# Performance work log

Hardware: AMD Instinct MI355X
Metric: run time of the kernel (lower is better)

## Reference

```python
import jax, jax.numpy as jnp
import numpy as np

N = 3072          # num nodes
E = 49152         # num edges (avg degree 16)
D = 256           # hidden_dim
O = 512           # output_dim
H = 8             # num_heads
DH = D // H       # head_dim = 32
NET = 5           # num_edge_types
NC = 8            # num_communities
L_LOC = 2         # num_local_layers
L_GLB = 2         # num_global_layers


def _layernorm(x, g, b, eps=1e-5):
    m = jnp.mean(x, axis=-1, keepdims=True)
    v = jnp.mean((x - m) ** 2, axis=-1, keepdims=True)
    return (x - m) * jax.lax.rsqrt(v + eps) * g + b


def setup_inputs() -> dict:
    key = jax.random.key(0)
    ks = jax.random.split(key, 40)
    s = 0.02
    inp = {
        "x": jax.random.normal(ks[0], (N, 1), jnp.float32),
        "edge_index": jax.random.randint(ks[1], (2, E), 0, N),
        "edge_types": jax.random.randint(ks[2], (E,), 0, NET),
        "pos_encoding": jax.random.normal(ks[3], (N, D), jnp.float32),
        "community_ids": jax.random.randint(ks[4], (N,), 0, NC),
        "adj_matrix": jnp.zeros((N, N), jnp.float32),
        # node embedding Linear(1, D)
        "emb_w": jax.random.normal(ks[5], (1, D)) * s,
        "emb_b": jnp.zeros((D,)),
        # local (Graphormer) layers, stacked over L_LOC
        "loc_qw": jax.random.normal(ks[6], (L_LOC, D, D)) * s,
        "loc_qb": jnp.zeros((L_LOC, D)),
        "loc_kw": jax.random.normal(ks[7], (L_LOC, D, D)) * s,
        "loc_kb": jnp.zeros((L_LOC, D)),
        "loc_vw": jax.random.normal(ks[8], (L_LOC, D, D)) * s,
        "loc_vb": jnp.zeros((L_LOC, D)),
        "loc_ow": jax.random.normal(ks[9], (L_LOC, D, D)) * s,
        "loc_ob": jnp.zeros((L_LOC, D)),
        "loc_eb": jax.random.normal(ks[10], (L_LOC, NET, H)) * s,  # edge-type attn bias per head
        "loc_ln_g": jnp.ones((L_LOC, D)),
        "loc_ln_b": jnp.zeros((L_LOC, D)),
        # global interaction layers, stacked over L_GLB
        "glob_qw": jax.random.normal(ks[11], (L_GLB, D, D)) * s,
        "glob_qb": jnp.zeros((L_GLB, D)),
        "glob_kw": jax.random.normal(ks[12], (L_GLB, D, D)) * s,
        "glob_kb": jnp.zeros((L_GLB, D)),
        "glob_vw": jax.random.normal(ks[13], (L_GLB, D, D)) * s,
        "glob_vb": jnp.zeros((L_GLB, D)),
        "glob_ow": jax.random.normal(ks[14], (L_GLB, D, D)) * s,
        "glob_ob": jnp.zeros((L_GLB, D)),
        "glob_ln_g": jnp.ones((L_GLB, D)),
        "glob_ln_b": jnp.zeros((L_GLB, D)),
        # output projection
        "out_w": jax.random.normal(ks[15], (D, O)) * s,
        "out_b": jnp.zeros((O,)),
    }
    return inp


def reference(x, edge_index, edge_types, pos_encoding, community_ids, adj_matrix,
              emb_w, emb_b,
              loc_qw, loc_qb, loc_kw, loc_kb, loc_vw, loc_vb, loc_ow, loc_ob,
              loc_eb, loc_ln_g, loc_ln_b,
              glob_qw, glob_qb, glob_kw, glob_kb, glob_vw, glob_vb,
              glob_ow, glob_ob, glob_ln_g, glob_ln_b,
              out_w, out_b):
    n = x.shape[0]
    h = x @ emb_w + emb_b                                  # [N, D]
    same = community_ids[:, None] == community_ids[None, :]  # [N, N] same-community mask
    src, dst = edge_index[0], edge_index[1]

    # Local layers: the original per-community subgraph loop (with full attention
    # inside each community) is mathematically a single masked full attention
    # restricted to same-community pairs, with edge-type bias at graph edges.
    for l in range(loc_qw.shape[0]):
        hp = h + pos_encoding
        q = (hp @ loc_qw[l] + loc_qb[l]).reshape(n, H, DH)
        k = (hp @ loc_kw[l] + loc_kb[l]).reshape(n, H, DH)
        v = (hp @ loc_vw[l] + loc_vb[l]).reshape(n, H, DH)
        # edge-type attention bias, scattered at edges  -> [H, N, N]
        bias = jnp.zeros((H, n, n), dtype=h.dtype).at[:, src, dst].add(loc_eb[l][edge_types].T)
        scores = jnp.einsum('nhd,mhd->hnm', q, k) / np.sqrt(DH) + bias
        scores = jnp.where(same[None, :, :], scores, -jnp.inf)  # attend within community only
        attn = jax.nn.softmax(scores, axis=-1)
        o = jnp.einsum('hnm,mhd->nhd', attn, v).reshape(n, D)
        h = _layernorm(h + o @ loc_ow[l] + loc_ob[l], loc_ln_g[l], loc_ln_b[l])

    # Global interaction: attend only to nodes in *different* communities
    for g in range(glob_qw.shape[0]):
        Q = h @ glob_qw[g] + glob_qb[g]
        K = h @ glob_kw[g] + glob_kb[g]
        V = h @ glob_vw[g] + glob_vb[g]
        scores = (Q @ K.T) / np.sqrt(DH)                   # scaled by head_dim as in source
        scores = jnp.where(~same, scores, -jnp.inf)        # mask same-community (incl. self)
        attn = jax.nn.softmax(scores, axis=-1)
        o = (attn @ V) @ glob_ow[g] + glob_ob[g]
        h = _layernorm(o + h, glob_ln_g[g], glob_ln_b[g])

    return h @ out_w + out_b                               # [N, O]
```

## Files before the change

### kernel.cpp

```cpp
#include <hip/hip_runtime.h>
#include <hip/hip_bf16.h>
#include <stdint.h>

#define NN 3072
#define EE 49152
#define DD 256
#define OO 512
#define HH 8
#define DHH 32
#define NETT 5
#define NC 8
#define NCMAX 512
#define SCP 516
#define KS 16
#define NW 17

typedef __attribute__((ext_vector_type(8))) short short8;
typedef __attribute__((ext_vector_type(4))) float f32x4;

__device__ __forceinline__ short f2bf_s(float f){
    __hip_bfloat16 h = __float2bfloat16(f);
    return *reinterpret_cast<short*>(&h);
}
__device__ __forceinline__ float bf2f_s(short v){
    __hip_bfloat16 h;
    *reinterpret_cast<short*>(&h) = v;
    return __bfloat162float(h);
}

__global__ void k_embed(const float* __restrict__ x, const float* __restrict__ w,
                        const float* __restrict__ b, float* __restrict__ h){
    int i = blockIdx.x * 256 + threadIdx.x;
    int n = i >> 8, d = i & 255;
    h[i] = x[n] * w[d] + b[d];
}

__global__ __launch_bounds__(256) void k_vtrans(const float* __restrict__ v, short* __restrict__ vt){
    __shared__ float t[32][33];
    int bx = blockIdx.x;
    int by = blockIdx.y;
    int lx = threadIdx.x & 31, ly = threadIdx.x >> 5;
    for (int i = ly; i < 32; i += 8)
        t[i][lx] = v[(size_t)(bx * 32 + i) * DD + by * 32 + lx];
    __syncthreads();
    for (int r = ly; r < 32; r += 8)
        vt[(size_t)(by * 32 + r) * NN + bx * 32 + lx] = f2bf_s(t[lx][r]);
}

__global__ __launch_bounds__(256) void k_vtrans_sorted(const float* __restrict__ v,
                                                       const int* __restrict__ perm,
                                                       short* __restrict__ vt){
    __shared__ float t[32][33];
    int bx = blockIdx.x;
    int by = blockIdx.y;
    int lx = threadIdx.x & 31, ly = threadIdx.x >> 5;
    for (int i = ly; i < 32; i += 8)
        t[i][lx] = v[(size_t)perm[bx * 32 + i] * DD + by * 32 + lx];
    __syncthreads();
    for (int r = ly; r < 32; r += 8)
        vt[(size_t)(by * 32 + r) * NN + bx * 32 + lx] = f2bf_s(t[lx][r]);
}

struct WT {
    const float* src[NW];
    short*       dst[NW];
    int          M[NW];
};
__global__ __launch_bounds__(256) void k_wtrans(WT wt){
    int id = blockIdx.z;
    int M = wt.M[id];
    int bx = blockIdx.x;
    if (bx * 32 >= M) return;
    int by = blockIdx.y;
    __shared__ float t[32][33];
    int lx = threadIdx.x & 31, ly = threadIdx.x >> 5;
    const float* w = wt.src[id];
    for (int i = ly; i < 32; i += 8)
        t[i][lx] = w[(size_t)(by * 32 + i) * M + bx * 32 + lx];
    __syncthreads();
    short* d = wt.dst[id];
    for (int r = ly; r < 32; r += 8)
        d[(size_t)(bx * 32 + r) * DD + by * 32 + lx] = f2bf_s(t[lx][r]);
}

__global__ void k_count(const int* __restrict__ ei, int* __restrict__ cnt){
    int e = blockIdx.x * 256 + threadIdx.x;
    if (e < EE) atomicAdd(&cnt[ei[e]], 1);
}

__global__ void k_scan(const int* __restrict__ cnt, int* __restrict__ rp){
    __shared__ int part[256];
    int tid = threadIdx.x;
    int base = tid * 12;
    int loc[12]; int s = 0;
    for (int i = 0; i < 12; i++){ loc[i] = s; s += cnt[base + i]; }
    part[tid] = s; __syncthreads();
    if (tid == 0){ int a = 0; for (int i = 0; i < 256; i++){ int t = part[i]; part[i] = a; a += t; } }
    __syncthreads();
    int b = part[tid];
    for (int i = 0; i < 12; i++) rp[base + i] = b + loc[i];
    if (tid == 255) rp[NN] = b + s;
}

__global__ void k_fill(const int* __restrict__ ei, const int* __restrict__ et,
                       const int* __restrict__ rp, int* __restrict__ cur,
                       int* __restrict__ e_dst, int* __restrict__ e_typ){
    int e = blockIdx.x * 256 + threadIdx.x;
    if (e < EE){
        int s = ei[e], d = ei[EE + e];
        int p = atomicAdd(&cur[s], 1);
        int idx = rp[s] + p;
        e_dst[idx] = d; e_typ[idx] = et[e];
    }
}

__global__ void k_ccount(const int* __restrict__ comm, int* __restrict__ ccnt){
    int n = blockIdx.x * 256 + threadIdx.x;
    if (n < NN) atomicAdd(&ccnt[comm[n]], 1);
}

__global__ void k_cscan(const int* __restrict__ ccnt, int* __restrict__ cstart){
    cstart[0] = 0;
    for (int c = 0; c < NC; c++) cstart[c + 1] = cstart[c] + ccnt[c];
}

__global__ void k_cfill(const int* __restrict__ comm, const int* __restrict__ cstart,
                        int* __restrict__ ccur, int* __restrict__ perm, int* __restrict__ inv){
    int n = blockIdx.x * 256 + threadIdx.x;
    if (n < NN){
        int c = comm[n];
        int p = cstart[c] + atomicAdd(&ccur[c], 1);
        perm[p] = n; inv[n] = p;
    }
}

template<int M>
__global__ __launch_bounds__(256) void k_gemm_mfma(
        const float* __restrict__ A, const float* __restrict__ P,
        const short* __restrict__ Wt, const float* __restrict__ bias,
        float* __restrict__ C, short* __restrict__ Cbf){
    int tid = threadIdx.x;
    int w = tid >> 6, lane = tid & 63, quad = lane >> 4, col = lane & 15;
    int m0 = blockIdx.x * 64 + w * 16;
    int n0 = blockIdx.y * 64;

    const float* arow = A + (size_t)(m0 + col) * DD;
    const float* prow = P ? P + (size_t)(m0 + col) * DD : nullptr;

    f32x4 acc[4];
    #pragma unroll
    for (int su = 0; su < 4; su++) acc[su] = (f32x4){0.f, 0.f, 0.f, 0.f};

    #pragma unroll
    for (int f = 0; f < 8; f++){
        int k0 = f * 32 + quad * 8;
        float4 a0 = *(const float4*)(arow + k0);
        float4 a1 = *(const float4*)(arow + k0 + 4);
        if (P){
            float4 p0 = *(const float4*)(prow + k0);
            float4 p1 = *(const float4*)(prow + k0 + 4);
            a0.x += p0.x; a0.y += p0.y; a0.z += p0.z; a0.w += p0.w;
            a1.x += p1.x; a1.y += p1.y; a1.z += p1.z; a1.w += p1.w;
        }
        short8 af;
        af[0] = f2bf_s(a0.x); af[1] = f2bf_s(a0.y); af[2] = f2bf_s(a0.z); af[3] = f2bf_s(a0.w);
        af[4] = f2bf_s(a1.x); af[5] = f2bf_s(a1.y); af[6] = f2bf_s(a1.z); af[7] = f2bf_s(a1.w);
        #pragma unroll
        for (int su = 0; su < 4; su++){
            short8 bf = *(const short8*)(Wt + (size_t)(n0 + su * 16 + col) * DD + k0);
            acc[su] = __builtin_amdgcn_mfma_f32_16x16x32_bf16(af, bf, acc[su], 0, 0, 0);
        }
    }

    #pragma unroll
    for (int su = 0; su < 4; su++){
        int n = n0 + su * 16 + col;
        float bz = bias[n];
        #pragma unroll
        for (int r = 0; r < 4; r++){
            float val = acc[su][r] + bz;
            size_t idx = (size_t)(m0 + quad * 4 + r) * M + n;
            C[idx] = val;
            if (Cbf) Cbf[idx] = f2bf_s(val);
        }
    }
}

struct QKV {
    const short* Wt[3];
    const float* bias[3];
    float*       Cf[3];
    short*       Cb[3];
};
__global__ __launch_bounds__(256) void k_gemm_qkv(
        const float* __restrict__ A, const float* __restrict__ P,
        QKV q, const int* __restrict__ inv){
    int z = blockIdx.z;
    const short* Wt = q.Wt[z];
    const float* bias = q.bias[z];
    float* Cf = q.Cf[z];
    short* Cb = q.Cb[z];

    int tid = threadIdx.x;
    int w = tid >> 6, lane = tid & 63, quad = lane >> 4, col = lane & 15;
    int m0 = blockIdx.x * 64 + w * 16;
    int n0 = blockIdx.y * 64;

    const float* arow = A + (size_t)(m0 + col) * DD;
    const float* prow = P ? P + (size_t)(m0 + col) * DD : nullptr;

    f32x4 acc[4];
    #pragma unroll
    for (int su = 0; su < 4; su++) acc[su] = (f32x4){0.f, 0.f, 0.f, 0.f};

    #pragma unroll
    for (int f = 0; f < 8; f++){
        int k0 = f * 32 + quad * 8;
        float4 a0 = *(const float4*)(arow + k0);
        float4 a1 = *(const float4*)(arow + k0 + 4);
        if (P){
            float4 p0 = *(const float4*)(prow + k0);
            float4 p1 = *(const float4*)(prow + k0 + 4);
            a0.x += p0.x; a0.y += p0.y; a0.z += p0.z; a0.w += p0.w;
            a1.x += p1.x; a1.y += p1.y; a1.z += p1.z; a1.w += p1.w;
        }
        short8 af;
        af[0] = f2bf_s(a0.x); af[1] = f2bf_s(a0.y); af[2] = f2bf_s(a0.z); af[3] = f2bf_s(a0.w);
        af[4] = f2bf_s(a1.x); af[5] = f2bf_s(a1.y); af[6] = f2bf_s(a1.z); af[7] = f2bf_s(a1.w);
        #pragma unroll
        for (int su = 0; su < 4; su++){
            short8 bf = *(const short8*)(Wt + (size_t)(n0 + su * 16 + col) * DD + k0);
            acc[su] = __builtin_amdgcn_mfma_f32_16x16x32_bf16(af, bf, acc[su], 0, 0, 0);
        }
    }

    #pragma unroll
    for (int su = 0; su < 4; su++){
        int n = n0 + su * 16 + col;
        float bz = bias[n];
        #pragma unroll
        for (int r = 0; r < 4; r++){
            float val = acc[su][r] + bz;
            int m = m0 + quad * 4 + r;
            if (Cf) Cf[(size_t)m * DD + n] = val;
            if (Cb){
                int ms = inv ? inv[m] : m;
                Cb[(size_t)ms * DD + n] = f2bf_s(val);
            }
        }
    }
}

__global__ __launch_bounds__(256) void k_ln_res(float* __restrict__ h, const float* __restrict__ t,
                                                const float* __restrict__ g, const float* __restrict__ b){
    int n = blockIdx.x, d = threadIdx.x;
    __shared__ float red[256];
    float v = h[n * 256 + d] + t[n * 256 + d];
    red[d] = v; __syncthreads();
    for (int s = 128; s > 0; s >>= 1){ if (d < s) red[d] += red[d + s]; __syncthreads(); }
    float mean = red[0] * (1.0f / 256.0f); __syncthreads();
    float c = v - mean;
    red[d] = c * c; __syncthreads();
    for (int s = 128; s > 0; s >>= 1){ if (d < s) red[d] += red[d + s]; __syncthreads(); }
    float var = red[0] * (1.0f / 256.0f);
    h[n * 256 + d] = c * rsqrtf(var + 1e-5f) * g[d] + b[d];
}

__global__ __launch_bounds__(256) void k_local_attn6(
        const short* __restrict__ Qs, const short* __restrict__ Ks, const short* __restrict__ Vts,
        const int* __restrict__ cstart, const int* __restrict__ perm, const int* __restrict__ inv,
        const int* __restrict__ rp, const int* __restrict__ e_dst, const int* __restrict__ e_typ,
        const float* __restrict__ eb, float* __restrict__ o){
    int c  = blockIdx.y;
    int hh = blockIdx.z;
    int cs0 = cstart[c], cs1 = cstart[c + 1];
    int Nc = cs1 - cs0;
    int p0 = blockIdx.x * 16;
    if (p0 >= Nc) return;
    int tid = threadIdx.x;
    int w = tid >> 6, lane = tid & 63, quad = lane >> 4, col = lane & 15;
    int nt  = (Nc + 15) >> 4;
    int nt2 = (Nc + 31) >> 5;

    __shared__ float sc[16][SCP];
    __shared__ float linv[16];
    __shared__ int qnode[16];

    if (tid < 16) qnode[tid] = (p0 + tid < Nc) ? perm[cs0 + p0 + tid] : -1;

    int qrow = cs0 + min(p0 + col, Nc - 1);
    short8 qf = *(const short8*)(Qs + (size_t)qrow * DD + hh * DHH + quad * 8);

    const float scale = 0.17677669529663687f;

    for (int t = w; t < nt; t += 4){
        int kt = t * 16;
        int krow = cs0 + min(kt + col, Nc - 1);
        short8 kf = *(const short8*)(Ks + (size_t)krow * DD + hh * DHH + quad * 8);
        f32x4 s = __builtin_amdgcn_mfma_f32_16x16x32_bf16(qf, kf, (f32x4){0.f,0.f,0.f,0.f}, 0, 0, 0);
        #pragma unroll
        for (int r = 0; r < 4; r++)
            sc[quad * 4 + r][kt + col] = s[r] * scale;
    }
    __syncthreads();

    int qi = tid >> 4, l16 = tid & 15;
    {
        int n = qnode[qi];
        if (n >= 0){
            int re = rp[n + 1];
            for (int e2 = rp[n] + l16; e2 < re; e2 += 16){
                int dpos = inv[e_dst[e2]];
                if (dpos >= cs0 && dpos < cs1)
                    atomicAdd(&sc[qi][dpos - cs0], eb[e_typ[e2] * HH + hh]);
            }
        }
    }
    __syncthreads();

    {
        float lm = -1e30f;
        for (int m = l16; m < Nc; m += 16) lm = fmaxf(lm, sc[qi][m]);
        #pragma unroll
        for (int off = 1; off < 16; off <<= 1) lm = fmaxf(lm, __shfl_xor(lm, off));
        float ls = 0.f;
        for (int m = l16; m < Nc; m += 16){
            float e_ = __expf(sc[qi][m] - lm);
            sc[qi][m] = e_;
            ls += e_;
        }
        for (int m = (Nc & ~15) + l16; m < nt2 * 32; m += 16)
            if (m >= Nc) sc[qi][m] = 0.f;
        #pragma unroll
        for (int off = 1; off < 16; off <<= 1) ls += __shfl_xor(ls, off);
        if (l16 == 0) linv[qi] = 1.f / ls;
    }
    __syncthreads();

    f32x4 acc0 = (f32x4){0.f,0.f,0.f,0.f}, acc1 = (f32x4){0.f,0.f,0.f,0.f};
    for (int t2 = w; t2 < nt2; t2 += 4){
        int kt = t2 * 32;
        float4 pa = *(const float4*)&sc[col][kt + quad * 8];
        float4 pb = *(const float4*)&sc[col][kt + quad * 8 + 4];
        short8 pf;
        pf[0] = f2bf_s(pa.x); pf[1] = f2bf_s(pa.y); pf[2] = f2bf_s(pa.z); pf[3] = f2bf_s(pa.w);
        pf[4] = f2bf_s(pb.x); pf[5] = f2bf_s(pb.y); pf[6] = f2bf_s(pb.z); pf[7] = f2bf_s(pb.w);
        const short* vb0 = Vts + (size_t)(hh * DHH + col) * NN + cs0 + kt + quad * 8;
        short8 vf0 = *(const short8*)(vb0);
        short8 vf1 = *(const short8*)(vb0 + (size_t)16 * NN);
        acc0 = __builtin_amdgcn_mfma_f32_16x16x32_bf16(pf, vf0, acc0, 0, 0, 0);
        acc1 = __builtin_amdgcn_mfma_f32_16x16x32_bf16(pf, vf1, acc1, 0, 0, 0);
    }
    __syncthreads();
    {
        float (*pv)[16][33] = reinterpret_cast<float (*)[16][33]>(&sc[0][0]);
        #pragma unroll
        for (int r = 0; r < 4; r++){
            pv[w][quad * 4 + r][col]      = acc0[r];
            pv[w][quad * 4 + r][col + 16] = acc1[r];
        }
        __syncthreads();

        int q = tid >> 4, d0 = tid & 15;
        int n = qnode[q];
        #pragma unroll
        for (int half = 0; half < 2; half++){
            int dd = d0 + half * 16;
            float sum = pv[0][q][dd] + pv[1][q][dd] + pv[2][q][dd] + pv[3][q][dd];
            if (n >= 0) o[(size_t)n * DD + hh * DHH + dd] = sum * linv[q];
        }
    }
}

__global__ __launch_bounds__(256) void k_glob_mfma9(
        const short* __restrict__ Qb, const short* __restrict__ Kb,
        const short* __restrict__ Vt, const int* __restrict__ comm,
        short* __restrict__ Opart, float* __restrict__ lpart){
    int tid = threadIdx.x;
    int w = tid >> 6, lane = tid & 63, quad = lane >> 4, col = lane & 15;
    int qt = blockIdx.x * 64 + w * 16;
    int split = blockIdx.y;
    int ks0 = split * (NN / KS);

    __shared__ __align__(16) short Kl[32][264];
    __shared__ __align__(16) short Vl[256][40];
    __shared__ __align__(16) short Pl[4][16][40];

    short8 qf[8];
    #pragma unroll
    for (int f = 0; f < 8; f++)
        qf[f] = *(const short8*)(Qb + (size_t)(qt + col) * DD + f * 32 + quad * 8);

    int qc[4];
    #pragma unroll
    for (int r = 0; r < 4; r++) qc[r] = comm[qt + quad * 4 + r];

    f32x4 accO[16];
    #pragma unroll
    for (int dt = 0; dt < 16; dt++) accO[dt] = (f32x4){0.f, 0.f, 0.f, 0.f};
    float l_[4] = {0.f, 0.f, 0.f, 0.f};

    const float scale = 0.17677669529663687f;

    for (int t = 0; t < NN / KS / 32; t++){
        int kt = ks0 + t * 32;
        __syncthreads();
        #pragma unroll
        for (int i = 0; i < 4; i++){
            int idx = tid + i * 256;
            int row = idx >> 5, seg = idx & 31;
            *(short8*)&Kl[row][seg * 8] = *(const short8*)(Kb + (size_t)(kt + row) * DD + seg * 8);
        }
        #pragma unroll
        for (int i = 0; i < 4; i++){
            int idx = tid + i * 256;
            int d = idx >> 2, seg = idx & 3;
            *(short8*)&Vl[d][seg * 8] = *(const short8*)(Vt + (size_t)d * NN + kt + seg * 8);
        }
        __syncthreads();

        f32x4 s0 = (f32x4){0.f,0.f,0.f,0.f}, s1 = (f32x4){0.f,0.f,0.f,0.f};
        #pragma unroll
        for (int f = 0; f < 8; f++){
            short8 kf0 = *(const short8*)&Kl[col][f * 32 + quad * 8];
            short8 kf1 = *(const short8*)&Kl[16 + col][f * 32 + quad * 8];
            s0 = __builtin_amdgcn_mfma_f32_16x16x32_bf16(qf[f], kf0, s0, 0, 0, 0);
            s1 = __builtin_amdgcn_mfma_f32_16x16x32_bf16(qf[f], kf1, s1, 0, 0, 0);
        }

        int cm0 = comm[kt + col], cm1 = comm[kt + 16 + col];
        #pragma unroll
        for (int r = 0; r < 4; r++){
            float p0 = (cm0 != qc[r]) ? __expf(s0[r] * scale) : 0.f;
            float p1 = (cm1 != qc[r]) ? __expf(s1[r] * scale) : 0.f;
            l_[r] += p0 + p1;
            int row = quad * 4 + r;
            Pl[w][row][col]      = f2bf_s(p0);
            Pl[w][row][col + 16] = f2bf_s(p1);
        }
        short8 pf = *(const short8*)(&Pl[w][col][quad * 8]);
        #pragma unroll
        for (int dt = 0; dt < 16; dt++){
            short8 vf = *(const short8*)&Vl[dt * 16 + col][quad * 8];
            accO[dt] = __builtin_amdgcn_mfma_f32_16x16x32_bf16(pf, vf, accO[dt], 0, 0, 0);
        }
    }

    #pragma unroll
    for (int r = 0; r < 4; r++){
        float vv = l_[r];
        #pragma unroll
        for (int off = 1; off < 16; off <<= 1) vv += __shfl_xor(vv, off);
        l_[r] = vv;
    }

    #pragma unroll
    for (int r = 0; r < 4; r++){
        int row = qt + quad * 4 + r;
        if (col == 0) lpart[split * NN + row] = l_[r];
        #pragma unroll
        for (int dt = 0; dt < 16; dt++)
            Opart[((size_t)split * NN + row) * DD + dt * 16 + col] = f2bf_s(accO[dt][r]);
    }
}

__global__ __launch_bounds__(256) void k_gmerge(
        const short* __restrict__ Opart, const float* __restrict__ lpart,
        float* __restrict__ o){
    int qn = blockIdx.x, d = threadIdx.x;
    float l = 0.f, val = 0.f;
    #pragma unroll
    for (int s = 0; s < KS; s++){
        l += lpart[s * NN + qn];
        val += bf2f_s(Opart[((size_t)s * NN + qn) * DD + d]);
    }
    o[(size_t)qn * DD + d] = val / l;
}

extern "C" void kernel_launch(void* const* d_in, const int* in_sizes, int n_in,
                              void* d_out, int out_size, void* d_ws, size_t ws_size,
                              hipStream_t stream){
    const float* x        = (const float*)d_in[0];
    const int*   ei       = (const int*)  d_in[1];
    const int*   et       = (const int*)  d_in[2];
    const float* pos      = (const float*)d_in[3];
    const int*   comm     = (const int*)  d_in[4];
    const float* emb_w    = (const float*)d_in[6];
    const float* emb_b    = (const float*)d_in[7];
    const float* loc_qw   = (const float*)d_in[8];
    const float* loc_qb   = (const float*)d_in[9];
    const float* loc_kw   = (const float*)d_in[10];
    const float* loc_kb   = (const float*)d_in[11];
    const float* loc_vw   = (const float*)d_in[12];
    const float* loc_vb   = (const float*)d_in[13];
    const float* loc_ow   = (const float*)d_in[14];
    const float* loc_ob   = (const float*)d_in[15];
    const float* loc_eb   = (const float*)d_in[16];
    const float* loc_ln_g = (const float*)d_in[17];
    const float* loc_ln_b = (const float*)d_in[18];
    const float* glob_qw  = (const float*)d_in[19];
    const float* glob_qb  = (const float*)d_in[20];
    const float* glob_kw  = (const float*)d_in[21];
    const float* glob_kb  = (const float*)d_in[22];
    const float* glob_vw  = (const float*)d_in[23];
    const float* glob_vb  = (const float*)d_in[24];
    const float* glob_ow  = (const float*)d_in[25];
    const float* glob_ob  = (const float*)d_in[26];
    const float* glob_ln_g= (const float*)d_in[27];
    const float* glob_ln_b= (const float*)d_in[28];
    const float* out_w    = (const float*)d_in[29];
    const float* out_b    = (const float*)d_in[30];

    float* h    = (float*)d_ws;
    float* qb_  = h    + NN * DD;
    float* kb_  = qb_  + NN * DD;
    float* vb_  = kb_  + NN * DD;
    float* ob_  = vb_  + NN * DD;
    float* tb_  = ob_  + NN * DD;
    float* lpart= tb_  + NN * DD;
    int* cnt    = (int*)(lpart + KS * NN);
    int* cur    = cnt + NN;
    int* ccnt   = cur + NN;
    int* ccur   = ccnt + NC;
    int* cstart = ccur + NC;
    int* rp     = cstart + NC + 1;
    int* perm   = rp + NN + 1;
    int* inv    = perm + NN;
    int* e_dst  = inv + NN;
    int* e_typ  = e_dst + EE;
    short* Qbf  = (short*)(((uintptr_t)(e_typ + EE) + 15) & ~(uintptr_t)15);
    short* Kbf  = Qbf + NN * DD;
    short* Vt   = Kbf + NN * DD;
    short* WtAll= Vt + (size_t)DD * NN;
    short* Qs   = WtAll + 16 * DD * DD + DD * OO;
    short* Ks2  = Qs + (size_t)NN * DD;
    short* Vts  = Ks2 + (size_t)NN * DD;
    short* Opart= Vts + (size_t)DD * NN;

    WT wt;
    const float* wsrc[NW] = {
        loc_qw, loc_kw, loc_vw, loc_ow,
        loc_qw + DD * DD, loc_kw + DD * DD, loc_vw + DD * DD, loc_ow + DD * DD,
        glob_qw, glob_kw, glob_vw, glob_ow,
        glob_qw + DD * DD, glob_kw + DD * DD, glob_vw + DD * DD, glob_ow + DD * DD,
        out_w };
    for (int i = 0; i < NW; i++){
        wt.src[i] = wsrc[i];
        wt.dst[i] = WtAll + (size_t)i * DD * DD;
        wt.M[i]   = (i == 16) ? OO : DD;
    }
    short* WtLQ[2] = { WtAll + 0 * DD * DD, WtAll + 4 * DD * DD };
    short* WtLK[2] = { WtAll + 1 * DD * DD, WtAll + 5 * DD * DD };
    short* WtLV[2] = { WtAll + 2 * DD * DD, WtAll + 6 * DD * DD };
    short* WtLO[2] = { WtAll + 3 * DD * DD, WtAll + 7 * DD * DD };
    short* WtGQ[2] = { WtAll + 8 * DD * DD, WtAll + 12 * DD * DD };
    short* WtGK[2] = { WtAll + 9 * DD * DD, WtAll + 13 * DD * DD };
    short* WtGV[2] = { WtAll + 10 * DD * DD, WtAll + 14 * DD * DD };
    short* WtGO[2] = { WtAll + 11 * DD * DD, WtAll + 15 * DD * DD };
    short* WtOut   = WtAll + 16 * DD * DD;

    (void)hipMemsetAsync(cnt, 0, sizeof(int) * (2 * NN + 2 * NC), stream);

    k_embed<<<NN * DD / 256, 256, 0, stream>>>(x, emb_w, emb_b, h);
    k_wtrans<<<dim3(16, 8, NW), 256, 0, stream>>>(wt);
    k_count<<<EE / 256, 256, 0, stream>>>(ei, cnt);
    k_scan<<<1, 256, 0, stream>>>(cnt, rp);
    k_fill<<<EE / 256, 256, 0, stream>>>(ei, et, rp, cur, e_dst, e_typ);
    k_ccount<<<NN / 256, 256, 0, stream>>>(comm, ccnt);
    k_cscan<<<1, 1, 0, stream>>>(ccnt, cstart);
    k_cfill<<<NN / 256, 256, 0, stream>>>(comm, cstart, ccur, perm, inv);

    for (int l = 0; l < 2; l++){
        QKV q;
        q.Wt[0] = WtLQ[l]; q.Wt[1] = WtLK[l]; q.Wt[2] = WtLV[l];
        q.bias[0] = loc_qb + l * DD; q.bias[1] = loc_kb + l * DD; q.bias[2] = loc_vb + l * DD;
        q.Cf[0] = nullptr; q.Cf[1] = nullptr; q.Cf[2] = vb_;
        q.Cb[0] = Qs; q.Cb[1] = Ks2; q.Cb[2] = nullptr;
        k_gemm_qkv<<<dim3(NN / 64, DD / 64, 3), 256, 0, stream>>>(h, pos, q, inv);
        k_vtrans_sorted<<<dim3(NN / 32, DD / 32), 256, 0, stream>>>(vb_, perm, Vts);
        k_local_attn6<<<dim3(NCMAX / 16, NC, HH), 256, 0, stream>>>(
            Qs, Ks2, Vts, cstart, perm, inv, rp, e_dst, e_typ,
            loc_eb + l * NETT * HH, ob_);
        k_gemm_mfma<DD><<<dim3(NN / 64, DD / 64), 256, 0, stream>>>(ob_, nullptr, WtLO[l], loc_ob + l * DD, tb_, nullptr);
        k_ln_res<<<NN, 256, 0, stream>>>(h, tb_, loc_ln_g + l * DD, loc_ln_b + l * DD);
    }

    for (int g = 0; g < 2; g++){
        QKV q;
        q.Wt[0] = WtGQ[g]; q.Wt[1] = WtGK[g]; q.Wt[2] = WtGV[g];
        q.bias[0] = glob_qb + g * DD; q.bias[1] = glob_kb + g * DD; q.bias[2] = glob_vb + g * DD;
        q.Cf[0] = nullptr; q.Cf[1] = nullptr; q.Cf[2] = vb_;
        q.Cb[0] = Qbf; q.Cb[1] = Kbf; q.Cb[2] = nullptr;
        k_gemm_qkv<<<dim3(NN / 64, DD / 64, 3), 256, 0, stream>>>(h, nullptr, q, nullptr);
        k_vtrans<<<dim3(NN / 32, DD / 32), 256, 0, stream>>>(vb_, Vt);
        k_glob_mfma9<<<dim3(NN / 64, KS), 256, 0, stream>>>(Qbf, Kbf, Vt, comm, Opart, lpart);
        k_gmerge<<<NN, 256, 0, stream>>>(Opart, lpart, ob_);
        k_gemm_mfma<DD><<<dim3(NN / 64, DD / 64), 256, 0, stream>>>(ob_, nullptr, WtGO[g], glob_ob + g * DD, tb_, nullptr);
        k_ln_res<<<NN, 256, 0, stream>>>(h, tb_, glob_ln_g + g * DD, glob_ln_b + g * DD);
    }

    k_gemm_mfma<OO><<<dim3(NN / 64, OO / 64), 256, 0, stream>>>(h, nullptr, WtOut, out_b, (float*)d_out, nullptr);
}
```

Before: 518.2 us.

## Fuse output projection with residual LayerNorm and keep activations in bf16

The output-projection GEMM and the residual LayerNorm now run in one kernel. Each block computes a full 16-row slice of 256 columns, stages it in shared memory and normalises it with shuffle reductions. The embedding and LN kernels also write bf16 copies of h and of h+pos, and the attention outputs are stored as bf16, so the GEMMs load bf16 directly instead of converting fp32. This removes four LN launches plus their fp32 round trips and the per-GEMM conversion work. The cost is fewer blocks for the O-projection (192 blocks of 16 rows), which may lower occupancy.

```diff
diff --git a/kernel.cpp b/kernel.cpp
--- a/kernel.cpp
+++ b/kernel.cpp
@@ -29,10 +29,14 @@
 }
 
 __global__ void k_embed(const float* __restrict__ x, const float* __restrict__ w,
-                        const float* __restrict__ b, float* __restrict__ h){
+                        const float* __restrict__ b, const float* __restrict__ pos,
+                        float* __restrict__ h, short* __restrict__ hbf, short* __restrict__ hpbf){
     int i = blockIdx.x * 256 + threadIdx.x;
     int n = i >> 8, d = i & 255;
-    h[i] = x[n] * w[d] + b[d];
+    float v = x[n] * w[d] + b[d];
+    h[i] = v;
+    hbf[i] = f2bf_s(v);
+    hpbf[i] = f2bf_s(v + pos[i]);
 }
 
 __global__ __launch_bounds__(256) void k_vtrans(const float* __restrict__ v, short* __restrict__ vt){
@@ -136,16 +140,14 @@
 
 template<int M>
 __global__ __launch_bounds__(256) void k_gemm_mfma(
-        const float* __restrict__ A, const float* __restrict__ P,
-        const short* __restrict__ Wt, const float* __restrict__ bias,
-        float* __restrict__ C, short* __restrict__ Cbf){
+        const short* __restrict__ A, const short* __restrict__ Wt,
+        const float* __restrict__ bias, float* __restrict__ C){
     int tid = threadIdx.x;
     int w = tid >> 6, lane = tid & 63, quad = lane >> 4, col = lane & 15;
     int m0 = blockIdx.x * 64 + w * 16;
     int n0 = blockIdx.y * 64;
 
-    const float* arow = A + (size_t)(m0 + col) * DD;
-    const float* prow = P ? P + (size_t)(m0 + col) * DD : nullptr;
+    const short* arow = A + (size_t)(m0 + col) * DD;
 
     f32x4 acc[4];
     #pragma unroll
@@ -154,17 +156,7 @@
     #pragma unroll
     for (int f = 0; f < 8; f++){
         int k0 = f * 32 + quad * 8;
-        float4 a0 = *(const float4*)(arow + k0);
-        float4 a1 = *(const float4*)(arow + k0 + 4);
-        if (P){
-            float4 p0 = *(const float4*)(prow + k0);
-            float4 p1 = *(const float4*)(prow + k0 + 4);
-            a0.x += p0.x; a0.y += p0.y; a0.z += p0.z; a0.w += p0.w;
-            a1.x += p1.x; a1.y += p1.y; a1.z += p1.z; a1.w += p1.w;
-        }
-        short8 af;
-        af[0] = f2bf_s(a0.x); af[1] = f2bf_s(a0.y); af[2] = f2bf_s(a0.z); af[3] = f2bf_s(a0.w);
-        af[4] = f2bf_s(a1.x); af[5] = f2bf_s(a1.y); af[6] = f2bf_s(a1.z); af[7] = f2bf_s(a1.w);
+        short8 af = *(const short8*)(arow + k0);
         #pragma unroll
         for (int su = 0; su < 4; su++){
             short8 bf = *(const short8*)(Wt + (size_t)(n0 + su * 16 + col) * DD + k0);
@@ -177,12 +169,8 @@
         int n = n0 + su * 16 + col;
         float bz = bias[n];
         #pragma unroll
-        for (int r = 0; r < 4; r++){
-            float val = acc[su][r] + bz;
-            size_t idx = (size_t)(m0 + quad * 4 + r) * M + n;
-            C[idx] = val;
-            if (Cbf) Cbf[idx] = f2bf_s(val);
-        }
+        for (int r = 0; r < 4; r++)
+            C[(size_t)(m0 + quad * 4 + r) * M + n] = acc[su][r] + bz;
     }
 }
 
@@ -193,8 +181,7 @@
     short*       Cb[3];
 };
 __global__ __launch_bounds__(256) void k_gemm_qkv(
-        const float* __restrict__ A, const float* __restrict__ P,
-        QKV q, const int* __restrict__ inv){
+        const short* __restrict__ A, QKV q, const int* __restrict__ inv){
     int z = blockIdx.z;
     const short* Wt = q.Wt[z];
     const float* bias = q.bias[z];
@@ -206,8 +193,7 @@
     int m0 = blockIdx.x * 64 + w * 16;
     int n0 = blockIdx.y * 64;
 
-    const float* arow = A + (size_t)(m0 + col) * DD;
-    const float* prow = P ? P + (size_t)(m0 + col) * DD : nullptr;
+    const short* arow = A + (size_t)(m0 + col) * DD;
 
     f32x4 acc[4];
     #pragma unroll
@@ -216,17 +202,7 @@
     #pragma unroll
     for (int f = 0; f < 8; f++){
         int k0 = f * 32 + quad * 8;
-        float4 a0 = *(const float4*)(arow + k0);
-        float4 a1 = *(const float4*)(arow + k0 + 4);
-        if (P){
-            float4 p0 = *(const float4*)(prow + k0);
-            float4 p1 = *(const float4*)(prow + k0 + 4);
-            a0.x += p0.x; a0.y += p0.y; a0.z += p0.z; a0.w += p0.w;
-            a1.x += p1.x; a1.y += p1.y; a1.z += p1.z; a1.w += p1.w;
-        }
-        short8 af;
-        af[0] = f2bf_s(a0.x); af[1] = f2bf_s(a0.y); af[2] = f2bf_s(a0.z); af[3] = f2bf_s(a0.w);
-        af[4] = f2bf_s(a1.x); af[5] = f2bf_s(a1.y); af[6] = f2bf_s(a1.z); af[7] = f2bf_s(a1.w);
+        short8 af = *(const short8*)(arow + k0);
         #pragma unroll
         for (int su = 0; su < 4; su++){
             short8 bf = *(const short8*)(Wt + (size_t)(n0 + su * 16 + col) * DD + k0);
@@ -251,26 +227,80 @@
     }
 }
 
-__global__ __launch_bounds__(256) void k_ln_res(float* __restrict__ h, const float* __restrict__ t,
-                                                const float* __restrict__ g, const float* __restrict__ b){
-    int n = blockIdx.x, d = threadIdx.x;
-    __shared__ float red[256];
-    float v = h[n * 256 + d] + t[n * 256 + d];
-    red[d] = v; __syncthreads();
-    for (int s = 128; s > 0; s >>= 1){ if (d < s) red[d] += red[d + s]; __syncthreads(); }
-    float mean = red[0] * (1.0f / 256.0f); __syncthreads();
-    float c = v - mean;
-    red[d] = c * c; __syncthreads();
-    for (int s = 128; s > 0; s >>= 1){ if (d < s) red[d] += red[d + s]; __syncthreads(); }
-    float var = red[0] * (1.0f / 256.0f);
-    h[n * 256 + d] = c * rsqrtf(var + 1e-5f) * g[d] + b[d];
+__global__ __launch_bounds__(256) void k_gemm_o_ln(
+        const short* __restrict__ A, const short* __restrict__ Wt,
+        const float* __restrict__ bias,
+        const float* __restrict__ g, const float* __restrict__ b,
+        const float* __restrict__ pos,
+        float* __restrict__ h, short* __restrict__ hbf, short* __restrict__ hpbf){
+    __shared__ float t[16][258];
+    int tid = threadIdx.x;
+    int w = tid >> 6, lane = tid & 63, quad = lane >> 4, col = lane & 15;
+    int m0 = blockIdx.x * 16;
+    int n0 = w * 64;
+
+    const short* arow = A + (size_t)(m0 + col) * DD;
+
+    f32x4 acc[4];
+    #pragma unroll
+    for (int su = 0; su < 4; su++) acc[su] = (f32x4){0.f, 0.f, 0.f, 0.f};
+
+    #pragma unroll
+    for (int f = 0; f < 8; f++){
+        int k0 = f * 32 + quad * 8;
+        short8 af = *(const short8*)(arow + k0);
+        #pragma unroll
+        for (int su = 0; su < 4; su++){
+            short8 bf = *(const short8*)(Wt + (size_t)(n0 + su * 16 + col) * DD + k0);
+            acc[su] = __builtin_amdgcn_mfma_f32_16x16x32_bf16(af, bf, acc[su], 0, 0, 0);
+        }
+    }
+
+    #pragma unroll
+    for (int su = 0; su < 4; su++){
+        int n = n0 + su * 16 + col;
+        float bz = bias[n];
+        #pragma unroll
+        for (int r = 0; r < 4; r++)
+            t[quad * 4 + r][n] = acc[su][r] + bz;
+    }
+    __syncthreads();
+
+    int row = tid >> 4, l16 = tid & 15;
+    int m = m0 + row;
+    float v[16];
+    float s = 0.f;
+    #pragma unroll
+    for (int j = 0; j < 16; j++){
+        int d = l16 + j * 16;
+        float vv = t[row][d] + h[(size_t)m * DD + d];
+        v[j] = vv; s += vv;
+    }
+    #pragma unroll
+    for (int off = 1; off < 16; off <<= 1) s += __shfl_xor(s, off);
+    float mean = s * (1.0f / 256.0f);
+    float s2 = 0.f;
+    #pragma unroll
+    for (int j = 0; j < 16; j++){ float c = v[j] - mean; s2 += c * c; }
+    #pragma unroll
+    for (int off = 1; off < 16; off <<= 1) s2 += __shfl_xor(s2, off);
+    float rstd = rsqrtf(s2 * (1.0f / 256.0f) + 1e-5f);
+    #pragma unroll
+    for (int j = 0; j < 16; j++){
+        int d = l16 + j * 16;
+        float out = (v[j] - mean) * rstd * g[d] + b[d];
+        size_t idx = (size_t)m * DD + d;
+        h[idx] = out;
+        hbf[idx] = f2bf_s(out);
+        if (pos) hpbf[idx] = f2bf_s(out + pos[idx]);
+    }
 }
 
 __global__ __launch_bounds__(256) void k_local_attn6(
         const short* __restrict__ Qs, const short* __restrict__ Ks, const short* __restrict__ Vts,
         const int* __restrict__ cstart, const int* __restrict__ perm, const int* __restrict__ inv,
         const int* __restrict__ rp, const int* __restrict__ e_dst, const int* __restrict__ e_typ,
-        const float* __restrict__ eb, float* __restrict__ o){
+        const float* __restrict__ eb, short* __restrict__ obbf){
     int c  = blockIdx.y;
     int hh = blockIdx.z;
     int cs0 = cstart[c], cs1 = cstart[c + 1];
@@ -367,7 +397,7 @@
         for (int half = 0; half < 2; half++){
             int dd = d0 + half * 16;
             float sum = pv[0][q][dd] + pv[1][q][dd] + pv[2][q][dd] + pv[3][q][dd];
-            if (n >= 0) o[(size_t)n * DD + hh * DHH + dd] = sum * linv[q];
+            if (n >= 0) obbf[(size_t)n * DD + hh * DHH + dd] = f2bf_s(sum * linv[q]);
         }
     }
 }
@@ -466,7 +496,7 @@
 
 __global__ __launch_bounds__(256) void k_gmerge(
         const short* __restrict__ Opart, const float* __restrict__ lpart,
-        float* __restrict__ o){
+        short* __restrict__ obbf){
     int qn = blockIdx.x, d = threadIdx.x;
     float l = 0.f, val = 0.f;
     #pragma unroll
@@ -474,7 +504,7 @@
         l += lpart[s * NN + qn];
         val += bf2f_s(Opart[((size_t)s * NN + qn) * DD + d]);
     }
-    o[(size_t)qn * DD + d] = val / l;
+    obbf[(size_t)qn * DD + d] = f2bf_s(val / l);
 }
 
 extern "C" void kernel_launch(void* const* d_in, const int* in_sizes, int n_in,
@@ -512,12 +542,8 @@
     const float* out_b    = (const float*)d_in[30];
 
     float* h    = (float*)d_ws;
-    float* qb_  = h    + NN * DD;
-    float* kb_  = qb_  + NN * DD;
-    float* vb_  = kb_  + NN * DD;
-    float* ob_  = vb_  + NN * DD;
-    float* tb_  = ob_  + NN * DD;
-    float* lpart= tb_  + NN * DD;
+    float* vb_  = h    + NN * DD;
+    float* lpart= vb_  + NN * DD;
     int* cnt    = (int*)(lpart + KS * NN);
     int* cur    = cnt + NN;
     int* ccnt   = cur + NN;
@@ -536,6 +562,9 @@
     short* Ks2  = Qs + (size_t)NN * DD;
     short* Vts  = Ks2 + (size_t)NN * DD;
     short* Opart= Vts + (size_t)DD * NN;
+    short* hbf  = Opart + (size_t)KS * NN * DD;
+    short* hpbf = hbf + (size_t)NN * DD;
+    short* obbf = hpbf + (size_t)NN * DD;
 
     WT wt;
     const float* wsrc[NW] = {
@@ -561,7 +590,7 @@
 
     (void)hipMemsetAsync(cnt, 0, sizeof(int) * (2 * NN + 2 * NC), stream);
 
-    k_embed<<<NN * DD / 256, 256, 0, stream>>>(x, emb_w, emb_b, h);
+    k_embed<<<NN * DD / 256, 256, 0, stream>>>(x, emb_w, emb_b, pos, h, hbf, hpbf);
     k_wtrans<<<dim3(16, 8, NW), 256, 0, stream>>>(wt);
     k_count<<<EE / 256, 256, 0, stream>>>(ei, cnt);
     k_scan<<<1, 256, 0, stream>>>(cnt, rp);
@@ -576,13 +605,14 @@
         q.bias[0] = loc_qb + l * DD; q.bias[1] = loc_kb + l * DD; q.bias[2] = loc_vb + l * DD;
         q.Cf[0] = nullptr; q.Cf[1] = nullptr; q.Cf[2] = vb_;
         q.Cb[0] = Qs; q.Cb[1] = Ks2; q.Cb[2] = nullptr;
-        k_gemm_qkv<<<dim3(NN / 64, DD / 64, 3), 256, 0, stream>>>(h, pos, q, inv);
+        k_gemm_qkv<<<dim3(NN / 64, DD / 64, 3), 256, 0, stream>>>(hpbf, q, inv);
         k_vtrans_sorted<<<dim3(NN / 32, DD / 32), 256, 0, stream>>>(vb_, perm, Vts);
         k_local_attn6<<<dim3(NCMAX / 16, NC, HH), 256, 0, stream>>>(
             Qs, Ks2, Vts, cstart, perm, inv, rp, e_dst, e_typ,
-            loc_eb + l * NETT * HH, ob_);
-        k_gemm_mfma<DD><<<dim3(NN / 64, DD / 64), 256, 0, stream>>>(ob_, nullptr, WtLO[l], loc_ob + l * DD, tb_, nullptr);
-        k_ln_res<<<NN, 256, 0, stream>>>(h, tb_, loc_ln_g + l * DD, loc_ln_b + l * DD);
+            loc_eb + l * NETT * HH, obbf);
+        k_gemm_o_ln<<<NN / 16, 256, 0, stream>>>(
+            obbf, WtLO[l], loc_ob + l * DD, loc_ln_g + l * DD, loc_ln_b + l * DD,
+            (l == 0) ? pos : nullptr, h, hbf, hpbf);
     }
 
     for (int g = 0; g < 2; g++){
@@ -591,13 +621,14 @@
         q.bias[0] = glob_qb + g * DD; q.bias[1] = glob_kb + g * DD; q.bias[2] = glob_vb + g * DD;
         q.Cf[0] = nullptr; q.Cf[1] = nullptr; q.Cf[2] = vb_;
         q.Cb[0] = Qbf; q.Cb[1] = Kbf; q.Cb[2] = nullptr;
-        k_gemm_qkv<<<dim3(NN / 64, DD / 64, 3), 256, 0, stream>>>(h, nullptr, q, nullptr);
+        k_gemm_qkv<<<dim3(NN / 64, DD / 64, 3), 256, 0, stream>>>(hbf, q, nullptr);
         k_vtrans<<<dim3(NN / 32, DD / 32), 256, 0, stream>>>(vb_, Vt);
         k_glob_mfma9<<<dim3(NN / 64, KS), 256, 0, stream>>>(Qbf, Kbf, Vt, comm, Opart, lpart);
-        k_gmerge<<<NN, 256, 0, stream>>>(Opart, lpart, ob_);
-        k_gemm_mfma<DD><<<dim3(NN / 64, DD / 64), 256, 0, stream>>>(ob_, nullptr, WtGO[g], glob_ob + g * DD, tb_, nullptr);
-        k_ln_res<<<NN, 256, 0, stream>>>(h, tb_, glob_ln_g + g * DD, glob_ln_b + g * DD);
-    }
-
-    k_gemm_mfma<OO><<<dim3(NN / 64, OO / 64), 256, 0, stream>>>(h, nullptr, WtOut, out_b, (float*)d_out, nullptr);
-}
+        k_gmerge<<<NN, 256, 0, stream>>>(Opart, lpart, obbf);
+        k_gemm_o_ln<<<NN / 16, 256, 0, stream>>>(
+            obbf, WtGO[g], glob_ob + g * DD, glob_ln_g + g * DD, glob_ln_b + g * DD,
+            nullptr, h, hbf, nullptr);
+    }
+
+    k_gemm_mfma<OO><<<dim3(NN / 64, OO / 64), 256, 0, stream>>>(hbf, WtOut, out_b, (float*)d_out);
+}
```

New measurement: 503.7 us. 2.8% less time.
